# Optimization experiments

Measured on AMD Instinct MI355X. Metric: run time of the kernel, lower is better.

Reference implementation:

```python
import jax, jax.numpy as jnp
import numpy as np

B, S, HID, LAYERS, HEADS, WINDOW = 2, 4096, 768, 4, 12, 256
W = WINDOW // 2            # one-sided window: each token attends to W left, W right
HD = HID // HEADS          # head dim = 64
MAXPOS = (S // WINDOW + 1) * WINDOW + 1
EPS = 1e-12                # Longformer layer_norm_eps


def layer_norm(x, g, b):
    m = x.mean(-1, keepdims=True)
    v = ((x - m) ** 2).mean(-1, keepdims=True)
    return (x - m) * jax.lax.rsqrt(v + EPS) * g + b


def sliding_window_attention(q, k, v, key_mask):
    # q,k,v: [B,H,S,D]; key_mask: [B,S] bool. Band attention: |i-j| <= W.
    Bz, Hh, Sl, D = q.shape
    nC = Sl // W
    q = q / jnp.sqrt(jnp.asarray(D, q.dtype))
    cidx = jnp.arange(nC)[:, None] + jnp.arange(3)[None, :]            # [nC,3] chunk gather
    kp = jnp.pad(k, ((0, 0), (0, 0), (W, W), (0, 0))).reshape(Bz, Hh, nC + 2, W, D)
    vp = jnp.pad(v, ((0, 0), (0, 0), (W, W), (0, 0))).reshape(Bz, Hh, nC + 2, W, D)
    kw = kp[:, :, cidx].reshape(Bz, Hh, nC, 3 * W, D)                  # keys for each query chunk
    vw = vp[:, :, cidx].reshape(Bz, Hh, nC, 3 * W, D)
    qc = q.reshape(Bz, Hh, nC, W, D)
    scores = jnp.einsum('bhcqd,bhckd->bhcqk', qc, kw)                  # [B,H,nC,W,3W]
    p = jnp.arange(W)[:, None]
    j = jnp.arange(3 * W)[None, :]
    band = (j >= p) & (j <= p + 2 * W)                                  # [W,3W] banded validity
    keypos = jnp.arange(nC)[:, None, None] * W + j[None] - W           # [nC,1,3W] global key idx
    inrange = (keypos >= 0) & (keypos < Sl)
    kmw = jnp.pad(key_mask, ((0, 0), (W, W))).reshape(Bz, nC + 2, W)[:, cidx].reshape(Bz, nC, 3 * W)
    mask = (band[None] & inrange)[None, None] & kmw[:, None, :, None, :]
    scores = jnp.where(mask, scores, jnp.asarray(-1e9, scores.dtype))
    probs = jax.nn.softmax(scores, axis=-1)
    out = jnp.einsum('bhcqk,bhckd->bhcqd', probs, vw)
    return out.reshape(Bz, Hh, Sl, D)


def heads_split(x):
    return x.reshape(x.shape[0], x.shape[1], HEADS, HD).transpose(0, 2, 1, 3)


def heads_merge(x):
    return x.transpose(0, 2, 1, 3).reshape(x.shape[0], x.shape[2], HID)


def forward(embeddings, pos_emb, tok_emb, emb_ln_g, emb_ln_b, Wq, bq, Wk, bk, Wv, bv,
            Wo, bo, ln1_g, ln1_b, Wi, bi, Wf, bf, ln2_g, ln2_b, Wp, bp, attention_mask):
    Sl = embeddings.shape[1]
    # Longformer embeddings: inputs_embeds + absolute positions (padding_idx+1 .. ) + token type 0
    h = embeddings + pos_emb[1:Sl + 1][None] + tok_emb[0][None, None]
    h = layer_norm(h, emb_ln_g, emb_ln_b)
    km = attention_mask.astype(bool)
    for l in range(LAYERS):
        q = heads_split(h @ Wq[l] + bq[l])
        k = heads_split(h @ Wk[l] + bk[l])
        v = heads_split(h @ Wv[l] + bv[l])
        a = heads_merge(sliding_window_attention(q, k, v, km))
        h = layer_norm(h + (a @ Wo[l] + bo[l]), ln1_g[l], ln1_b[l])
        f = jax.nn.gelu(h @ Wi[l] + bi[l], approximate=False) @ Wf[l] + bf[l]
        h = layer_norm(h + f, ln2_g[l], ln2_b[l])
    return jax.nn.sigmoid((h @ Wp + bp).squeeze(-1))


def setup_inputs() -> dict:
    key = jax.random.key(0)
    ks = jax.random.split(key, 12)
    nrm = lambda k, sh: jax.random.normal(k, sh, jnp.float32) * 0.02
    return dict(
        embeddings=jax.random.normal(ks[0], (B, S, HID), jnp.float32),
        attention_mask=jnp.ones((B, S), jnp.int32),
        pos_emb=nrm(ks[1], (MAXPOS, HID)),
        tok_emb=nrm(ks[2], (2, HID)),
        emb_ln_g=jnp.ones((HID,), jnp.float32),
        emb_ln_b=jnp.zeros((HID,), jnp.float32),
        Wq=nrm(ks[3], (LAYERS, HID, HID)), bq=jnp.zeros((LAYERS, HID), jnp.float32),
        Wk=nrm(ks[4], (LAYERS, HID, HID)), bk=jnp.zeros((LAYERS, HID), jnp.float32),
        Wv=nrm(ks[5], (LAYERS, HID, HID)), bv=jnp.zeros((LAYERS, HID), jnp.float32),
        Wo=nrm(ks[6], (LAYERS, HID, HID)), bo=jnp.zeros((LAYERS, HID), jnp.float32),
        ln1_g=jnp.ones((LAYERS, HID), jnp.float32), ln1_b=jnp.zeros((LAYERS, HID), jnp.float32),
        Wi=nrm(ks[7], (LAYERS, HID, 4 * HID)), bi=jnp.zeros((LAYERS, 4 * HID), jnp.float32),
        Wf=nrm(ks[8], (LAYERS, 4 * HID, HID)), bf=jnp.zeros((LAYERS, HID), jnp.float32),
        ln2_g=jnp.ones((LAYERS, HID), jnp.float32), ln2_b=jnp.zeros((LAYERS, HID), jnp.float32),
        Wp=nrm(ks[9], (HID, 1)), bp=jnp.zeros((1,), jnp.float32),
    )


def reference(embeddings, attention_mask, pos_emb, tok_emb, emb_ln_g, emb_ln_b, Wq, bq, Wk, bk,
              Wv, bv, Wo, bo, ln1_g, ln1_b, Wi, bi, Wf, bf, ln2_g, ln2_b, Wp, bp):
    return forward(embeddings, pos_emb, tok_emb, emb_ln_g, emb_ln_b, Wq, bq, Wk, bk, Wv, bv,
                   Wo, bo, ln1_g, ln1_b, Wi, bi, Wf, bf, ln2_g, ln2_b, Wp, bp, attention_mask)
```

## Files before the change

kernel.cpp:

```cpp
#include <hip/hip_runtime.h>
#include <hip/hip_bf16.h>


typedef __bf16 bf16;
typedef bf16  bf16x4  __attribute__((ext_vector_type(4)));
typedef bf16  bf16x8  __attribute__((ext_vector_type(8)));
typedef float floatx4 __attribute__((ext_vector_type(4)));

#define MFMA16(a, b, c) __builtin_amdgcn_mfma_f32_16x16x32_bf16((a), (b), (c), 0, 0, 0)

__device__ __forceinline__ void gld_lds16(const bf16* gp, bf16* lp) {
  __builtin_amdgcn_global_load_lds(
      (const __attribute__((address_space(1))) void*)gp,
      (__attribute__((address_space(3))) void*)lp, 16, 0, 0);
}

__device__ __forceinline__ float fast_rcp(float x) {
  return __builtin_amdgcn_rcpf(x);
}

__device__ __forceinline__ float gelu_fast(float v) {
  float x2 = v * v;
  float u = __builtin_fmaf(x2, -0.07135481f, -1.59576912f);
  float e = __expf(v * u);
  return v * fast_rcp(1.f + e);
}

static constexpr size_t SZ_WTQKV = (size_t)4 * 2304 * 768 * 2;
static constexpr size_t SZ_WTO   = (size_t)4 * 768 * 768 * 2;
static constexpr size_t SZ_WTI   = (size_t)4 * 3072 * 768 * 2;
static constexpr size_t SZ_WTF   = (size_t)4 * 768 * 3072 * 2;
static constexpr size_t SZ_BQKV  = (size_t)4 * 2304 * 4;
static constexpr size_t SZ_H32   = (size_t)8192 * 768 * 4;
static constexpr size_t SZ_HBF   = (size_t)8192 * 768 * 2;
static constexpr size_t SZ_QKV   = (size_t)8192 * 2304 * 2;
static constexpr size_t SZ_ATTN  = (size_t)8192 * 768 * 2;
static constexpr size_t SZ_TMP   = (size_t)8192 * 768 * 4;

static constexpr size_t OFF_WTQKV = 0;
static constexpr size_t OFF_WTO   = OFF_WTQKV + SZ_WTQKV;
static constexpr size_t OFF_WTI   = OFF_WTO   + SZ_WTO;
static constexpr size_t OFF_WTF   = OFF_WTI   + SZ_WTI;
static constexpr size_t OFF_BQKV  = OFF_WTF   + SZ_WTF;
static constexpr size_t OFF_H32   = OFF_BQKV  + SZ_BQKV;
static constexpr size_t OFF_HBF   = OFF_H32   + SZ_H32;
static constexpr size_t OFF_QKV   = OFF_HBF   + SZ_HBF;
static constexpr size_t OFF_ATTN  = OFF_QKV   + SZ_QKV;
static constexpr size_t OFF_TMP   = OFF_ATTN  + SZ_ATTN;
static constexpr size_t OFF_FFN1  = OFF_TMP   + SZ_TMP;

__global__ __launch_bounds__(256) void transpose_cast(
    const float* __restrict__ src, bf16* __restrict__ dst,
    int K, int N, long sStride, long dStride) {
  __shared__ float tile[32][33];
  const int l = blockIdx.z;
  src += (long)l * sStride;
  dst += (long)l * dStride;
  const int n0 = blockIdx.x * 32, k0 = blockIdx.y * 32;
  const int tx = threadIdx.x, ty = threadIdx.y;
#pragma unroll
  for (int i = 0; i < 4; ++i)
    tile[ty + i * 8][tx] = src[(long)(k0 + ty + i * 8) * N + n0 + tx];
  __syncthreads();
#pragma unroll
  for (int i = 0; i < 4; ++i)
    dst[(long)(n0 + ty + i * 8) * K + k0 + tx] = (bf16)tile[tx][ty + i * 8];
}

__global__ void bias_concat(const float* __restrict__ bq, const float* __restrict__ bk,
                            const float* __restrict__ bv, float* __restrict__ bqkv) {
  int i = blockIdx.x * 256 + threadIdx.x;
  if (i >= 4 * 2304) return;
  int l = i / 2304, p = i % 2304;
  float v = (p < 768) ? bq[l * 768 + p]
          : (p < 1536) ? bk[l * 768 + p - 768] : bv[l * 768 + p - 1536];
  bqkv[i] = v;
}

__device__ __forceinline__ void block_stats(float s1, float s2, float* red,
                                            float& mean, float& inv) {
  const int lane = threadIdx.x & 63, wave = threadIdx.x >> 6;
#pragma unroll
  for (int off = 32; off > 0; off >>= 1) {
    s1 += __shfl_down(s1, off, 64);
    s2 += __shfl_down(s2, off, 64);
  }
  if (lane == 0) { red[wave] = s1; red[4 + wave] = s2; }
  __syncthreads();
  s1 = red[0] + red[1] + red[2] + red[3];
  s2 = red[4] + red[5] + red[6] + red[7];
  mean = s1 * (1.f / 768.f);
  float var = s2 * (1.f / 768.f) - mean * mean;
  inv = rsqrtf(var + 1e-12f);
}

__global__ __launch_bounds__(256) void embed_ln_kernel(
    const float* __restrict__ emb, const float* __restrict__ pos,
    const float* __restrict__ tok, const float* __restrict__ g,
    const float* __restrict__ bta, float* __restrict__ h32, bf16* __restrict__ hbf) {
  __shared__ float red[8];
  const long base = (long)blockIdx.x * 768;
  const int s = blockIdx.x & 4095;
  const int t = threadIdx.x;
  float x[3], s1 = 0.f, s2 = 0.f;
#pragma unroll
  for (int i = 0; i < 3; ++i) {
    int c = t + i * 256;
    float v = emb[base + c] + pos[(long)(s + 1) * 768 + c] + tok[c];
    x[i] = v; s1 += v; s2 += v * v;
  }
  float mean, inv;
  block_stats(s1, s2, red, mean, inv);
#pragma unroll
  for (int i = 0; i < 3; ++i) {
    int c = t + i * 256;
    float y = (x[i] - mean) * inv * g[c] + bta[c];
    h32[base + c] = y;
    hbf[base + c] = (bf16)y;
  }
}

__global__ __launch_bounds__(256) void add_ln_kernel(
    float* __restrict__ h32, const bf16* __restrict__ p0,
    const bf16* __restrict__ p1, const float* __restrict__ bias,
    const float* __restrict__ g, const float* __restrict__ bta,
    bf16* __restrict__ hbf) {
  __shared__ float red[8];
  const long base = (long)blockIdx.x * 768;
  const int t = threadIdx.x;
  float x[3], s1 = 0.f, s2 = 0.f;
#pragma unroll
  for (int i = 0; i < 3; ++i) {
    int c = t + i * 256;
    float v = h32[base + c] + (float)p0[base + c] + (float)p1[base + c] + bias[c];
    x[i] = v; s1 += v; s2 += v * v;
  }
  float mean, inv;
  block_stats(s1, s2, red, mean, inv);
#pragma unroll
  for (int i = 0; i < 3; ++i) {
    int c = t + i * 256;
    float y = (x[i] - mean) * inv * g[c] + bta[c];
    h32[base + c] = y;
    hbf[base + c] = (bf16)y;
  }
}

template <int MODE, int N, int LD>
__global__ __launch_bounds__(512, 4) void gemm_kernel(
    const bf16* __restrict__ A, const bf16* __restrict__ BT,
    const float* __restrict__ bias, void* __restrict__ C0, void* __restrict__ C1,
    bf16* __restrict__ vtout, int ksize) {
  __shared__ bf16 smem[16384];
  bf16* As = smem;
  bf16* Bs = smem + 8192;
  const int tid  = threadIdx.x;
  const int wave = tid >> 6, lane = tid & 63, l15 = lane & 15, quad = lane >> 4;
  const int wm = wave >> 2, wn = wave & 3;
  const long m0 = (long)blockIdx.x * 128;
  const int  n0 = blockIdx.y * 128;
  const int  k0 = blockIdx.z * ksize;

  floatx4 acc[4][2] = {};
  const int rowoff = tid >> 3;
  const int sc_sw = (tid & 7) ^ (rowoff & 7);
  const int fsw = l15 & 7;
  const bf16* Ag = A + m0 * LD + k0 + sc_sw * 8;
  const bf16* Bg = BT + (long)n0 * LD + k0 + sc_sw * 8;

  for (int kt = 0; kt < ksize; kt += 64) {
#pragma unroll
    for (int p = 0; p < 2; ++p) {
      const int row = p * 64 + rowoff;
      gld_lds16(Ag + (long)row * LD + kt, As + p * 4096 + wave * 512);
      gld_lds16(Bg + (long)row * LD + kt, Bs + p * 4096 + wave * 512);
    }
    __syncthreads();
#pragma unroll
    for (int kk = 0; kk < 2; ++kk) {
      const int ch = ((kk * 4 + quad) ^ fsw) * 8;
      bf16x8 af[4], bfr[2];
#pragma unroll
      for (int nt = 0; nt < 2; ++nt)
        bfr[nt] = *(const bf16x8*)&Bs[(wn * 32 + nt * 16 + l15) * 64 + ch];
#pragma unroll
      for (int mt = 0; mt < 4; ++mt)
        af[mt] = *(const bf16x8*)&As[(wm * 64 + mt * 16 + l15) * 64 + ch];
#pragma unroll
      for (int mt = 0; mt < 4; ++mt)
#pragma unroll
        for (int nt = 0; nt < 2; ++nt)
          acc[mt][nt] = MFMA16(af[mt], bfr[nt], acc[mt][nt]);
    }
    __syncthreads();
  }

  if (MODE == 1 && n0 >= 1536) {
    const int b = (int)(m0 >> 12);
    const int sbase = ((int)m0 & 4095) + wm * 64 + quad * 4;
#pragma unroll
    for (int nt = 0; nt < 2; ++nt) {
      const int ng = n0 + wn * 32 + nt * 16 + l15;
      const float bb = bias[ng];
      const int col = ng - 1536;
      bf16* dst = vtout + (((long)(b * 12 + (col >> 6)) * 64 + (col & 63)) << 12);
#pragma unroll
      for (int mt = 0; mt < 4; ++mt) {
        bf16x4 v4;
#pragma unroll
        for (int r = 0; r < 4; ++r) v4[r] = (bf16)(acc[mt][nt][r] + bb);
        *(bf16x4*)&dst[sbase + mt * 16] = v4;
      }
    }
    return;
  }

  bf16* Cg = (bf16*)((MODE == 0 && blockIdx.z != 0) ? C1 : C0);
#pragma unroll
  for (int h = 0; h < 2; ++h) {
    if (wm == h) {
#pragma unroll
      for (int mt = 0; mt < 4; ++mt)
#pragma unroll
        for (int nt = 0; nt < 2; ++nt) {
          const float bb = (MODE == 0) ? 0.f : bias[n0 + wn * 32 + nt * 16 + l15];
#pragma unroll
          for (int r = 0; r < 4; ++r) {
            float v = acc[mt][nt][r] + bb;
            if (MODE == 2) v = gelu_fast(v);
            smem[(mt * 16 + quad * 4 + r) * 136 + wn * 32 + nt * 16 + l15] = (bf16)v;
          }
        }
    }
    __syncthreads();
    {
      const int row = tid >> 3;
#pragma unroll
      for (int p = 0; p < 2; ++p) {
        const int chunk = (tid & 7) + p * 8;
        bf16x8 vv = *(const bf16x8*)&smem[row * 136 + chunk * 8];
        *(bf16x8*)&Cg[(m0 + h * 64 + row) * N + n0 + chunk * 8] = vv;
      }
    }
    __syncthreads();
  }
}

__global__ __launch_bounds__(256) void attn_kernel(
    const bf16* __restrict__ qkv, const bf16* __restrict__ vt,
    const int* __restrict__ amask, bf16* __restrict__ attn_out) {
  constexpr int S = 4096, HID3 = 2304;
  __shared__ bf16 Ss[64 * 328];
  __shared__ bf16 Ts[64 * 64];
  __shared__ float redm[64], reds[64];

  const int x = blockIdx.x, q0 = x * 64, h = blockIdx.y, b = blockIdx.z;
  const int tid = threadIdx.x, wave = tid >> 6, lane = tid & 63;
  const int l15 = lane & 15, quad = lane >> 4;
  const int rowoff = tid >> 3;
  const int sc_sw = (tid & 7) ^ (rowoff & 7);
  const int fsw = l15 & 7;
  const int t_lo = (x < 2) ? (2 - x) : 0;
  const int t_hi = (x > 61) ? (66 - x) : 5;

  const bf16* Qb = qkv + (long)b * S * HID3 + h * 64;
  const bf16* Kb = Qb + 768;
  const bf16* Vt_bh = vt + ((long)(b * 12 + h)) * 64 * 4096;

  bf16x8 qf[2];
  {
    const long qrow = q0 + wave * 16 + l15;
    qf[0] = *(const bf16x8*)&Qb[qrow * HID3 + quad * 8];
    qf[1] = *(const bf16x8*)&Qb[qrow * HID3 + 32 + quad * 8];
  }

  float mrow[4] = {-3e38f, -3e38f, -3e38f, -3e38f};

  for (int t = t_lo; t < t_hi; ++t) {
    const int j0 = (x - 2 + t) * 64;
    __syncthreads();
#pragma unroll
    for (int p = 0; p < 2; ++p) {
      const int key = p * 32 + rowoff;
      gld_lds16(Kb + (long)(j0 + key) * HID3 + sc_sw * 8, &Ts[p * 2048 + wave * 512]);
    }
    __syncthreads();
    floatx4 sacc[4] = {};
#pragma unroll
    for (int kk = 0; kk < 2; ++kk) {
      const int ch = ((kk * 4 + quad) ^ fsw) * 8;
#pragma unroll
      for (int nt = 0; nt < 4; ++nt) {
        bf16x8 kf = *(const bf16x8*)&Ts[(nt * 16 + l15) * 64 + ch];
        sacc[nt] = MFMA16(qf[kk], kf, sacc[nt]);
      }
    }
#pragma unroll
    for (int nt = 0; nt < 4; ++nt) {
      const int jj = t * 64 + nt * 16 + l15;
      const int j = j0 + nt * 16 + l15;
      const bool jv = (amask[b * S + j] != 0);
#pragma unroll
      for (int r = 0; r < 4; ++r) {
        const int qi = wave * 16 + quad * 4 + r;
        const bool ok = jv && (jj >= qi) && (jj <= qi + 256);
        const float sv = ok ? sacc[nt][r] * 0.125f : -1e9f;
        mrow[r] = fmaxf(mrow[r], sv);
        Ss[(wave * 16 + quad * 4 + r) * 328 + jj] = (bf16)sv;
      }
    }
  }
#pragma unroll
  for (int off = 1; off < 16; off <<= 1)
#pragma unroll
    for (int r = 0; r < 4; ++r)
      mrow[r] = fmaxf(mrow[r], __shfl_xor(mrow[r], off, 64));
  if (l15 == 0) {
#pragma unroll
    for (int r = 0; r < 4; ++r) redm[wave * 16 + quad * 4 + r] = mrow[r];
  }
  __syncthreads();

  {
    const int row = wave * 16 + l15;
    const float mx = redm[row];
    float sum = 0.f;
    for (int c = t_lo * 8 + quad; c < t_hi * 8; c += 4) {
      bf16x8 pv = *(const bf16x8*)&Ss[row * 328 + c * 8];
#pragma unroll
      for (int u = 0; u < 8; ++u) {
        const float p = __expf((float)pv[u] - mx);
        sum += p;
        pv[u] = (bf16)p;
      }
      *(bf16x8*)&Ss[row * 328 + c * 8] = pv;
    }
    sum += __shfl_xor(sum, 16, 64);
    sum += __shfl_xor(sum, 32, 64);
    if (quad == 0) reds[row] = sum;
  }
  __syncthreads();

  floatx4 oacc[4] = {};
  for (int t = t_lo; t < t_hi; ++t) {
    const int j0 = (x - 2 + t) * 64;
    __syncthreads();
#pragma unroll
    for (int p = 0; p < 2; ++p) {
      const int d = p * 32 + rowoff;
      gld_lds16(Vt_bh + (long)d * 4096 + j0 + sc_sw * 8, &Ts[p * 2048 + wave * 512]);
    }
    __syncthreads();
#pragma unroll
    for (int kk = 0; kk < 2; ++kk) {
      const int ko = kk * 32 + quad * 8;
      const int ch = ((kk * 4 + quad) ^ fsw) * 8;
      bf16x8 pf = *(const bf16x8*)&Ss[(wave * 16 + l15) * 328 + t * 64 + ko];
#pragma unroll
      for (int nt = 0; nt < 4; ++nt) {
        bf16x8 vf = *(const bf16x8*)&Ts[(nt * 16 + l15) * 64 + ch];
        oacc[nt] = MFMA16(pf, vf, oacc[nt]);
      }
    }
  }

  float inv[4];
#pragma unroll
  for (int r = 0; r < 4; ++r) inv[r] = fast_rcp(reds[wave * 16 + quad * 4 + r]);
  const long orow = (long)b * S + q0 + wave * 16 + quad * 4;
#pragma unroll
  for (int nt = 0; nt < 4; ++nt)
#pragma unroll
    for (int r = 0; r < 4; ++r)
      attn_out[(orow + r) * 768 + h * 64 + nt * 16 + l15] =
          (bf16)(oacc[nt][r] * inv[r]);
}

__global__ __launch_bounds__(256) void final_kernel(
    const float* __restrict__ h32, const float* __restrict__ Wp,
    const float* __restrict__ bp, float* __restrict__ out) {
  const int wave = threadIdx.x >> 6, lane = threadIdx.x & 63;
  const long tok = (long)blockIdx.x * 4 + wave;
  float s = 0.f;
#pragma unroll
  for (int i = 0; i < 12; ++i) {
    const int c = lane + i * 64;
    s += h32[tok * 768 + c] * Wp[c];
  }
#pragma unroll
  for (int off = 32; off > 0; off >>= 1) s += __shfl_down(s, off, 64);
  if (lane == 0) out[tok] = fast_rcp(1.f + __expf(-(s + bp[0])));
}

extern "C" void kernel_launch(void* const* d_in, const int* in_sizes, int n_in,
                              void* d_out, int out_size, void* d_ws, size_t ws_size,
                              hipStream_t stream) {
  const float* emb   = (const float*)d_in[0];
  const int*   amask = (const int*)d_in[1];
  const float* pos   = (const float*)d_in[2];
  const float* tok   = (const float*)d_in[3];
  const float* elng  = (const float*)d_in[4];
  const float* elnb  = (const float*)d_in[5];
  const float* Wq = (const float*)d_in[6];   const float* bq = (const float*)d_in[7];
  const float* Wk = (const float*)d_in[8];   const float* bk = (const float*)d_in[9];
  const float* Wv = (const float*)d_in[10];  const float* bv = (const float*)d_in[11];
  const float* Wo = (const float*)d_in[12];  const float* bo = (const float*)d_in[13];
  const float* ln1g = (const float*)d_in[14]; const float* ln1b = (const float*)d_in[15];
  const float* Wi = (const float*)d_in[16];  const float* bi = (const float*)d_in[17];
  const float* Wf = (const float*)d_in[18];  const float* bfb = (const float*)d_in[19];
  const float* ln2g = (const float*)d_in[20]; const float* ln2b = (const float*)d_in[21];
  const float* Wp = (const float*)d_in[22];  const float* bp = (const float*)d_in[23];
  float* out = (float*)d_out;

  char* ws = (char*)d_ws;
  bf16*  WTqkv = (bf16*)(ws + OFF_WTQKV);
  bf16*  WTo   = (bf16*)(ws + OFF_WTO);
  bf16*  WTi   = (bf16*)(ws + OFF_WTI);
  bf16*  WTf   = (bf16*)(ws + OFF_WTF);
  float* bqkv  = (float*)(ws + OFF_BQKV);
  float* h32   = (float*)(ws + OFF_H32);
  bf16*  hbf   = (bf16*)(ws + OFF_HBF);
  bf16*  qkvb  = (bf16*)(ws + OFF_QKV);
  bf16*  part1 = (bf16*)(ws + OFF_QKV);
  bf16*  attnb = (bf16*)(ws + OFF_ATTN);
  bf16*  part0 = (bf16*)(ws + OFF_TMP);
  bf16*  vtb   = (bf16*)(ws + OFF_TMP);
  bf16*  ffn1  = (bf16*)(ws + OFF_FFN1);

  const dim3 tb(32, 8, 1);
  transpose_cast<<<dim3(24, 24, 4), tb, 0, stream>>>(Wq, WTqkv,               768, 768,  (long)768 * 768,  (long)2304 * 768);
  transpose_cast<<<dim3(24, 24, 4), tb, 0, stream>>>(Wk, WTqkv + 768 * 768,   768, 768,  (long)768 * 768,  (long)2304 * 768);
  transpose_cast<<<dim3(24, 24, 4), tb, 0, stream>>>(Wv, WTqkv + 1536 * 768,  768, 768,  (long)768 * 768,  (long)2304 * 768);
  transpose_cast<<<dim3(24, 24, 4), tb, 0, stream>>>(Wo, WTo,                 768, 768,  (long)768 * 768,  (long)768 * 768);
  transpose_cast<<<dim3(96, 24, 4), tb, 0, stream>>>(Wi, WTi,                 768, 3072, (long)768 * 3072, (long)3072 * 768);
  transpose_cast<<<dim3(24, 96, 4), tb, 0, stream>>>(Wf, WTf,                 3072, 768, (long)3072 * 768, (long)768 * 3072);
  bias_concat<<<36, 256, 0, stream>>>(bq, bk, bv, bqkv);

  embed_ln_kernel<<<8192, 256, 0, stream>>>(emb, pos, tok, elng, elnb, h32, hbf);

  for (int l = 0; l < 4; ++l) {
    gemm_kernel<1, 2304, 768><<<dim3(64, 18, 1), 512, 0, stream>>>(
        hbf, WTqkv + (size_t)l * 2304 * 768, bqkv + l * 2304, qkvb, nullptr, vtb, 768);
    attn_kernel<<<dim3(64, 12, 2), 256, 0, stream>>>(qkvb, vtb, amask, attnb);
    gemm_kernel<0, 768, 768><<<dim3(64, 6, 2), 512, 0, stream>>>(
        attnb, WTo + (size_t)l * 768 * 768, nullptr, part0, part1, nullptr, 384);
    add_ln_kernel<<<8192, 256, 0, stream>>>(h32, part0, part1, bo + l * 768,
                                            ln1g + l * 768, ln1b + l * 768, hbf);
    gemm_kernel<2, 3072, 768><<<dim3(64, 24, 1), 512, 0, stream>>>(
        hbf, WTi + (size_t)l * 3072 * 768, bi + l * 3072, ffn1, nullptr, nullptr, 768);
    gemm_kernel<0, 768, 3072><<<dim3(64, 6, 2), 512, 0, stream>>>(
        ffn1, WTf + (size_t)l * 768 * 3072, nullptr, part0, part1, nullptr, 1536);
    add_ln_kernel<<<8192, 256, 0, stream>>>(h32, part0, part1, bfb + l * 768,
                                            ln2g + l * 768, ln2b + l * 768, hbf);
  }

  final_kernel<<<2048, 256, 0, stream>>>(h32, Wp, bp, out);
}
```

Measured before the change: 1.088 ms.

## Use 4-wave GEMM blocks with 64x64 per-wave tiles and per-wave epilogue

The GEMM kernel drops from 8 waves to 4 waves per 128x128 block. Each wave now computes a 64x64 tile with 16 accumulators instead of 64x32, which raises register-level reuse of the A fragments. The epilogue now stages each 16-row strip through a private per-wave LDS region and writes it out without block-wide barriers, replacing the two-phase synchronized store. The cost is higher register pressure and fewer waves available to hide load latency.

```diff
diff --git a/kernel.cpp b/kernel.cpp
--- a/kernel.cpp
+++ b/kernel.cpp
@@ -147,21 +147,20 @@
 }
 
 template <int MODE, int N, int LD>
-__global__ __launch_bounds__(512, 4) void gemm_kernel(
+__global__ __launch_bounds__(256, 4) void gemm_kernel(
     const bf16* __restrict__ A, const bf16* __restrict__ BT,
     const float* __restrict__ bias, void* __restrict__ C0, void* __restrict__ C1,
     bf16* __restrict__ vtout, int ksize) {
-  __shared__ bf16 smem[16384];
-  bf16* As = smem;
-  bf16* Bs = smem + 8192;
+  __shared__ bf16 As[128 * 64];
+  __shared__ bf16 Bs[128 * 64];
   const int tid  = threadIdx.x;
   const int wave = tid >> 6, lane = tid & 63, l15 = lane & 15, quad = lane >> 4;
-  const int wm = wave >> 2, wn = wave & 3;
+  const int wm = wave >> 1, wn = wave & 1;
   const long m0 = (long)blockIdx.x * 128;
   const int  n0 = blockIdx.y * 128;
   const int  k0 = blockIdx.z * ksize;
 
-  floatx4 acc[4][2] = {};
+  floatx4 acc[4][4] = {};
   const int rowoff = tid >> 3;
   const int sc_sw = (tid & 7) ^ (rowoff & 7);
   const int fsw = l15 & 7;
@@ -170,27 +169,31 @@
 
   for (int kt = 0; kt < ksize; kt += 64) {
 #pragma unroll
-    for (int p = 0; p < 2; ++p) {
-      const int row = p * 64 + rowoff;
-      gld_lds16(Ag + (long)row * LD + kt, As + p * 4096 + wave * 512);
-      gld_lds16(Bg + (long)row * LD + kt, Bs + p * 4096 + wave * 512);
+    for (int p = 0; p < 4; ++p) {
+      const int row = p * 32 + rowoff;
+      gld_lds16(Ag + (long)row * LD + kt, As + p * 2048 + wave * 512);
+      gld_lds16(Bg + (long)row * LD + kt, Bs + p * 2048 + wave * 512);
     }
     __syncthreads();
 #pragma unroll
     for (int kk = 0; kk < 2; ++kk) {
       const int ch = ((kk * 4 + quad) ^ fsw) * 8;
-      bf16x8 af[4], bfr[2];
-#pragma unroll
-      for (int nt = 0; nt < 2; ++nt)
-        bfr[nt] = *(const bf16x8*)&Bs[(wn * 32 + nt * 16 + l15) * 64 + ch];
+      bf16x8 af[4];
 #pragma unroll
       for (int mt = 0; mt < 4; ++mt)
         af[mt] = *(const bf16x8*)&As[(wm * 64 + mt * 16 + l15) * 64 + ch];
 #pragma unroll
-      for (int mt = 0; mt < 4; ++mt)
+      for (int nh = 0; nh < 2; ++nh) {
+        bf16x8 bfr[2];
 #pragma unroll
         for (int nt = 0; nt < 2; ++nt)
-          acc[mt][nt] = MFMA16(af[mt], bfr[nt], acc[mt][nt]);
+          bfr[nt] = *(const bf16x8*)&Bs[(wn * 64 + nh * 32 + nt * 16 + l15) * 64 + ch];
+#pragma unroll
+        for (int mt = 0; mt < 4; ++mt)
+#pragma unroll
+          for (int nt = 0; nt < 2; ++nt)
+            acc[mt][nh * 2 + nt] = MFMA16(af[mt], bfr[nt], acc[mt][nh * 2 + nt]);
+      }
     }
     __syncthreads();
   }
@@ -199,8 +202,8 @@
     const int b = (int)(m0 >> 12);
     const int sbase = ((int)m0 & 4095) + wm * 64 + quad * 4;
 #pragma unroll
-    for (int nt = 0; nt < 2; ++nt) {
-      const int ng = n0 + wn * 32 + nt * 16 + l15;
+    for (int nt = 0; nt < 4; ++nt) {
+      const int ng = n0 + wn * 64 + nt * 16 + l15;
       const float bb = bias[ng];
       const int col = ng - 1536;
       bf16* dst = vtout + (((long)(b * 12 + (col >> 6)) * 64 + (col & 63)) << 12);
@@ -216,33 +219,26 @@
   }
 
   bf16* Cg = (bf16*)((MODE == 0 && blockIdx.z != 0) ? C1 : C0);
-#pragma unroll
-  for (int h = 0; h < 2; ++h) {
-    if (wm == h) {
-#pragma unroll
-      for (int mt = 0; mt < 4; ++mt)
-#pragma unroll
-        for (int nt = 0; nt < 2; ++nt) {
-          const float bb = (MODE == 0) ? 0.f : bias[n0 + wn * 32 + nt * 16 + l15];
-#pragma unroll
-          for (int r = 0; r < 4; ++r) {
-            float v = acc[mt][nt][r] + bb;
-            if (MODE == 2) v = gelu_fast(v);
-            smem[(mt * 16 + quad * 4 + r) * 136 + wn * 32 + nt * 16 + l15] = (bf16)v;
-          }
-        }
-    }
-    __syncthreads();
-    {
-      const int row = tid >> 3;
-#pragma unroll
-      for (int p = 0; p < 2; ++p) {
-        const int chunk = (tid & 7) + p * 8;
-        bf16x8 vv = *(const bf16x8*)&smem[row * 136 + chunk * 8];
-        *(bf16x8*)&Cg[(m0 + h * 64 + row) * N + n0 + chunk * 8] = vv;
-      }
-    }
-    __syncthreads();
+  bf16* Es = As + wave * 1152;
+#pragma unroll
+  for (int mt = 0; mt < 4; ++mt) {
+#pragma unroll
+    for (int nt = 0; nt < 4; ++nt) {
+      const float bb = (MODE == 0) ? 0.f : bias[n0 + wn * 64 + nt * 16 + l15];
+#pragma unroll
+      for (int r = 0; r < 4; ++r) {
+        float v = acc[mt][nt][r] + bb;
+        if (MODE == 2) v = gelu_fast(v);
+        Es[(quad * 4 + r) * 72 + nt * 16 + l15] = (bf16)v;
+      }
+    }
+#pragma unroll
+    for (int p = 0; p < 2; ++p) {
+      const int rr = p * 8 + (lane >> 3);
+      const int cc = (lane & 7) * 8;
+      bf16x8 vv = *(const bf16x8*)&Es[rr * 72 + cc];
+      *(bf16x8*)&Cg[(m0 + wm * 64 + mt * 16 + rr) * N + n0 + wn * 64 + cc] = vv;
+    }
   }
 }
 
@@ -439,16 +435,16 @@
   embed_ln_kernel<<<8192, 256, 0, stream>>>(emb, pos, tok, elng, elnb, h32, hbf);
 
   for (int l = 0; l < 4; ++l) {
-    gemm_kernel<1, 2304, 768><<<dim3(64, 18, 1), 512, 0, stream>>>(
+    gemm_kernel<1, 2304, 768><<<dim3(64, 18, 1), 256, 0, stream>>>(
         hbf, WTqkv + (size_t)l * 2304 * 768, bqkv + l * 2304, qkvb, nullptr, vtb, 768);
     attn_kernel<<<dim3(64, 12, 2), 256, 0, stream>>>(qkvb, vtb, amask, attnb);
-    gemm_kernel<0, 768, 768><<<dim3(64, 6, 2), 512, 0, stream>>>(
+    gemm_kernel<0, 768, 768><<<dim3(64, 6, 2), 256, 0, stream>>>(
         attnb, WTo + (size_t)l * 768 * 768, nullptr, part0, part1, nullptr, 384);
     add_ln_kernel<<<8192, 256, 0, stream>>>(h32, part0, part1, bo + l * 768,
                                             ln1g + l * 768, ln1b + l * 768, hbf);
-    gemm_kernel<2, 3072, 768><<<dim3(64, 24, 1), 512, 0, stream>>>(
+    gemm_kernel<2, 3072, 768><<<dim3(64, 24, 1), 256, 0, stream>>>(
         hbf, WTi + (size_t)l * 3072 * 768, bi + l * 3072, ffn1, nullptr, nullptr, 768);
-    gemm_kernel<0, 768, 3072><<<dim3(64, 6, 2), 512, 0, stream>>>(
+    gemm_kernel<0, 768, 3072><<<dim3(64, 6, 2), 256, 0, stream>>>(
         ffn1, WTf + (size_t)l * 768 * 3072, nullptr, part0, part1, nullptr, 1536);
     add_ln_kernel<<<8192, 256, 0, stream>>>(h32, part0, part1, bfb + l * 768,
                                             ln2g + l * 768, ln2b + l * 768, hbf);
```

Result: no change. 1.099 ms (+1.1%).
